# Optimization experiments

Hardware: AMD Instinct MI355X
Metric: run time of the kernel (lower is better)

Reference implementation:

```python
import math
import jax, jax.numpy as jnp
import numpy as np

B, T, DIN, D, L, H = 512, 16, 7, 512, 2, 8
FF = 4 * D
HD = D // H
NEG = -1e30


def setup_inputs() -> dict:
    key = jax.random.key(0)
    ks = jax.random.split(key, 18)
    s = 0.02
    n = lambda k, sh: jax.random.normal(k, sh, dtype=jnp.float32) * s
    return {
        "x_scalar_norm": jax.random.normal(ks[0], (B, T, DIN), dtype=jnp.float32),
        "ip_w": n(ks[1], (DIN, D)),   # input_proj (x @ W)
        "ip_b": n(ks[2], (D,)),
        "qkv_w": n(ks[3], (L, D, 3 * D)),  # packed in_proj per layer
        "qkv_b": n(ks[4], (L, 3 * D)),
        "out_w": n(ks[5], (L, D, D)),
        "out_b": n(ks[6], (L, D)),
        "ln1_s": jnp.ones((L, D), jnp.float32),
        "ln1_b": jnp.zeros((L, D), jnp.float32),
        "ff_w1": n(ks[7], (L, D, FF)),
        "ff_b1": n(ks[8], (L, FF)),
        "ff_w2": n(ks[9], (L, FF, D)),
        "ff_b2": n(ks[10], (L, D)),
        "ln2_s": jnp.ones((L, D), jnp.float32),
        "ln2_b": jnp.zeros((L, D), jnp.float32),
        "head_w": n(ks[11], (D, 3)),  # moment_head
        "head_b": n(ks[12], (3,)),
    }


def _pos_encoding(t, d):
    pos = jnp.arange(t, dtype=jnp.float32)[:, None]
    div = jnp.exp(jnp.arange(0, d, 2, dtype=jnp.float32) * (-math.log(10000.0) / d))
    pe = jnp.zeros((t, d), jnp.float32)
    pe = pe.at[:, 0::2].set(jnp.sin(pos * div))
    pe = pe.at[:, 1::2].set(jnp.cos(pos * div))
    return pe


def _ln(x, s, b, eps=1e-5):
    m = jnp.mean(x, axis=-1, keepdims=True)
    v = jnp.mean(jnp.square(x - m), axis=-1, keepdims=True)
    return (x - m) * jax.lax.rsqrt(v + eps) * s + b


def _encoder_layer(h, qkv_w, qkv_b, out_w, out_b, ln1_s, ln1_b,
                   w1, b1, w2, b2, ln2_s, ln2_b, causal):
    b, t, _ = h.shape
    qkv = h @ qkv_w + qkv_b  # [b, t, 3D]
    q, k, v = jnp.split(qkv, 3, axis=-1)
    q = q.reshape(b, t, H, HD).transpose(0, 2, 1, 3)  # bhqd
    k = k.reshape(b, t, H, HD).transpose(0, 2, 1, 3)
    v = v.reshape(b, t, H, HD).transpose(0, 2, 1, 3)
    scores = jnp.einsum('bhqd,bhkd->bhqk', q, k) / math.sqrt(HD)
    scores = jnp.where(causal[None, None], scores, NEG)
    attn = jax.nn.softmax(scores, axis=-1)
    o = jnp.einsum('bhqk,bhkd->bhqd', attn, v)
    o = o.transpose(0, 2, 1, 3).reshape(b, t, D) @ out_w + out_b
    h = _ln(h + o, ln1_s, ln1_b)           # post-norm (norm_first=False)
    ff = jax.nn.relu(h @ w1 + b1) @ w2 + b2
    return _ln(h + ff, ln2_s, ln2_b)


def reference(x_scalar_norm, ip_w, ip_b, qkv_w, qkv_b, out_w, out_b,
              ln1_s, ln1_b, ff_w1, ff_b1, ff_w2, ff_b2, ln2_s, ln2_b,
              head_w, head_b):
    b, t_total, _ = x_scalar_norm.shape
    pe = _pos_encoding(t_total, D)
    x_roll = x_scalar_norm
    preds = []
    for t in range(t_total):
        xp = x_roll[:, :t + 1, :]                 # full backbone recompute per step
        h = xp @ ip_w + ip_b + pe[None, :t + 1]
        causal = jnp.tril(jnp.ones((t + 1, t + 1), dtype=bool))
        for l in range(L):
            h = _encoder_layer(h, qkv_w[l], qkv_b[l], out_w[l], out_b[l],
                               ln1_s[l], ln1_b[l], ff_w1[l], ff_b1[l],
                               ff_w2[l], ff_b2[l], ln2_s[l], ln2_b[l], causal)
        y_t = h[:, -1, :] @ head_w + head_b       # [b, 3]
        preds.append(y_t)
        if t < t_total - 1:
            # eval mode: no teacher forcing; feed back detached prediction
            x_roll = x_roll.at[:, t + 1, DIN - 3:].set(jax.lax.stop_gradient(y_t))
    return jnp.stack(preds, axis=1)  # [b, T, 3]
```

## Files before the change

### kernel.cpp

```cpp
#include <hip/hip_runtime.h>
#include <hip/hip_bf16.h>
#include <math.h>


typedef __attribute__((__ext_vector_type__(8))) short short8;
typedef __attribute__((__ext_vector_type__(4))) float floatx4;

__device__ inline short8 as_short8(uint4 v){ union U{uint4 u; short8 s;} x; x.u=v; return x.s; }

__device__ inline ushort f2bf(float f){
    __hip_bfloat16 h = __float2bfloat16(f);
    ushort u; __builtin_memcpy(&u, &h, 2); return u;
}

__device__ inline uint32_t sld32(const void* p){
    return __hip_atomic_load((const uint32_t*)p, __ATOMIC_RELAXED, __HIP_MEMORY_SCOPE_SYSTEM);
}
__device__ inline void sst32(void* p, uint32_t v){
    __hip_atomic_store((uint32_t*)p, v, __ATOMIC_RELAXED, __HIP_MEMORY_SCOPE_SYSTEM);
}
__device__ inline unsigned long long sld64(const void* p){
    return __hip_atomic_load((const unsigned long long*)p, __ATOMIC_RELAXED, __HIP_MEMORY_SCOPE_SYSTEM);
}
__device__ inline void sst64(void* p, unsigned long long v){
    __hip_atomic_store((unsigned long long*)p, v, __ATOMIC_RELAXED, __HIP_MEMORY_SCOPE_SYSTEM);
}
__device__ inline float u2f(uint32_t u){ float f; __builtin_memcpy(&f, &u, 4); return f; }
__device__ inline uint32_t f2u(float f){ uint32_t u; __builtin_memcpy(&u, &f, 4); return u; }

#define WS_H      12582912
#define WS_TMP    13631488
#define WS_ST1    14680064
#define WS_ST2    14712832
#define WS_YPART  14745600
#define WS_BAR    14794752
#define WS_HBF    14796800
#define WS_ATTN   15321088
#define WS_FFBF   15845376
#define WS_KC     17942528
#define WS_VC     34719744

__global__ __launch_bounds__(256)
void swz_k(const float* __restrict__ qkv_w, const float* __restrict__ out_w,
           const float* __restrict__ ff1_w, const float* __restrict__ ff2_w,
           ushort* __restrict__ wsw)
{
    if (blockIdx.x == 0 && blockIdx.y == 0 && blockIdx.z == 0){
        unsigned* bar = (unsigned*)((char*)wsw + WS_BAR);
        for (int i = threadIdx.x; i < 512; i += 256)
            sst32(&bar[i], 0u);
    }
    int id = blockIdx.z; int l = id & 1; int mi = id >> 1;
    int K, N; const float* src; size_t doff;
    if (mi == 0)      { K = 512;  N = 1536; src = qkv_w + (size_t)l*786432;  doff = (size_t)l*786432; }
    else if (mi == 1) { K = 512;  N = 512;  src = out_w + (size_t)l*262144;  doff = 1572864 + (size_t)l*262144; }
    else if (mi == 2) { K = 512;  N = 2048; src = ff1_w + (size_t)l*1048576; doff = 2097152 + (size_t)l*1048576; }
    else              { K = 2048; N = 512;  src = ff2_w + (size_t)l*1048576; doff = 4194304 + (size_t)l*1048576; }
    int n0 = blockIdx.x * 64, k0 = blockIdx.y * 32;
    if (n0 >= N || k0 >= K) return;
    __shared__ float tt[32][64];
    int tid = threadIdx.x;
    int c = tid & 63, r = tid >> 6;
    #pragma unroll
    for (int i = 0; i < 8; ++i)
        tt[r + i*4][c] = src[(size_t)(k0 + r + i*4)*N + n0 + c];
    __syncthreads();
    int q = tid >> 6, n = tid & 63;
    union { ushort s[8]; uint4 v; } pk;
    #pragma unroll
    for (int i = 0; i < 8; ++i) pk.s[i] = f2bf(tt[q*8 + i][n]);
    ((uint4*)(wsw + doff))[(size_t)((k0 >> 5)*4 + q)*N + n0 + n] = pk.v;
}

#define ALDS(c, m) aLds[(((c) << 4)) + (((m) ^ ((c) & 15)))]

__global__ __launch_bounds__(512, 1)
void mega_k(const float* __restrict__ x, const float* __restrict__ ip_w,
            const float* __restrict__ ip_b, const float* __restrict__ qkv_b,
            const float* __restrict__ out_b, const float* __restrict__ ln1_s,
            const float* __restrict__ ln1_b, const float* __restrict__ ff_b1,
            const float* __restrict__ ff_b2, const float* __restrict__ ln2_s,
            const float* __restrict__ ln2_b, const float* __restrict__ hw,
            const float* __restrict__ hb, float* __restrict__ out,
            char* __restrict__ ws)
{
    const ushort* wsw = (const ushort*)ws;
    float* h     = (float*)(ws + WS_H);
    float* tmp   = (float*)(ws + WS_TMP);
    float* st1   = (float*)(ws + WS_ST1);
    float* st2   = (float*)(ws + WS_ST2);
    float* ypart = (float*)(ws + WS_YPART);
    unsigned* bar = (unsigned*)(ws + WS_BAR);
    __hip_bfloat16* hbf    = (__hip_bfloat16*)(ws + WS_HBF);
    __hip_bfloat16* attnbf = (__hip_bfloat16*)(ws + WS_ATTN);
    __hip_bfloat16* ffbf   = (__hip_bfloat16*)(ws + WS_FFBF);
    __hip_bfloat16* kc0    = (__hip_bfloat16*)(ws + WS_KC);
    __hip_bfloat16* vc0    = (__hip_bfloat16*)(ws + WS_VC);

    const int g  = blockIdx.x & 31;
    const int j  = blockIdx.x >> 5;
    const int b0 = g * 16;
    const int tid  = threadIdx.x;
    const int lane = tid & 63, w = tid >> 6;
    const int qd = lane >> 4, ln = lane & 15;
    unsigned* cnt = bar + g*16;
    unsigned epoch = 0;

    __shared__ uint4 aLds[256*16];
    __shared__ float qLds[16][68];
    __shared__ float yLds[16][3];
    __shared__ float meanLds[16], rstdLds[16];
    __shared__ float redS[4][4][4], redQ[4][4][4];
    __shared__ floatx4 fred[4][64];
    __shared__ float yred[4][16][3];

    auto gbar = [&]() {
        __syncthreads();
        epoch += 8;
        if (tid == 0){
            __hip_atomic_fetch_add(cnt, 1u, __ATOMIC_RELAXED, __HIP_MEMORY_SCOPE_SYSTEM);
            while (__hip_atomic_load(cnt, __ATOMIC_RELAXED, __HIP_MEMORY_SCOPE_SYSTEM) < epoch)
                __builtin_amdgcn_s_sleep(8);
        }
        __syncthreads();
    };

    for (int t = 0; t < 16; ++t){
        for (int l = 0; l < 2; ++l){
            __hip_bfloat16* kc = kc0 + (size_t)l*4194304;
            __hip_bfloat16* vc = vc0 + (size_t)l*4194304;

            if (l == 1){
                const unsigned long long* src = (const unsigned long long*)hbf;
                #pragma unroll
                for (int i = 0; i < 2; ++i){
                    int e = tid + i*512; int m = e >> 6, cg = e & 63;
                    size_t gi = ((size_t)(b0+m)*64 + cg)*2;
                    union { unsigned long long q[2]; uint4 v; } u;
                    u.q[0] = sld64(src + gi); u.q[1] = sld64(src + gi + 1);
                    ALDS(cg, m) = u.v;
                }
            } else {
                if (t > 0){
                    if (tid < 48){
                        int r = tid / 3, c = tid - r*3;
                        float yv = hb[c];
                        #pragma unroll
                        for (int jj = 0; jj < 8; ++jj)
                            yv += u2f(sld32(&ypart[((size_t)(b0+r)*8 + jj)*3 + c]));
                        yLds[r][c] = yv;
                        if (j == 0)
                            out[((size_t)(b0+r)*16 + (t-1))*3 + c] = yv;
                    }
                    __syncthreads();
                }
                #pragma unroll
                for (int i = 0; i < 2; ++i){
                    int e = tid + i*512; int m = e >> 6, cg = e & 63;
                    int b = b0 + m;
                    const float* xr = x + ((size_t)b*16 + t)*7;
                    float f4, f5, f6;
                    if (t == 0){ f4 = xr[4]; f5 = xr[5]; f6 = xr[6]; }
                    else { f4 = yLds[m][0]; f5 = yLds[m][1]; f6 = yLds[m][2]; }
                    float x0 = xr[0], x1 = xr[1], x2 = xr[2], x3 = xr[3];
                    float hv[8];
                    union { ushort s[8]; uint4 v; } pk;
                    #pragma unroll
                    for (int k = 0; k < 8; ++k){
                        int d = cg*8 + k;
                        int e2 = d & ~1;
                        float div = expf(-(float)e2 * (9.210340371976184f / 512.0f));
                        float arg = (float)t * div;
                        float pe = (d & 1) ? cosf(arg) : sinf(arg);
                        float acc = ip_b[d] + pe
                            + x0*ip_w[0*512+d] + x1*ip_w[1*512+d]
                            + x2*ip_w[2*512+d] + x3*ip_w[3*512+d]
                            + f4*ip_w[4*512+d] + f5*ip_w[5*512+d] + f6*ip_w[6*512+d];
                        hv[k] = acc;
                        pk.s[k] = f2bf(acc);
                    }
                    ALDS(cg, m) = pk.v;
                    if ((cg >> 3) == j){
                        float4* hp = (float4*)(h + (size_t)(b0+m)*512 + cg*8);
                        hp[0] = make_float4(hv[0],hv[1],hv[2],hv[3]);
                        hp[1] = make_float4(hv[4],hv[5],hv[6],hv[7]);
                    }
                }
            }
            __syncthreads();

            {
                const uint4* Bg = (const uint4*)(wsw + (size_t)l*786432);
                int s0 = (w < 4) ? (w >> 1) : 2;
                int cs = (w < 4) ? ((w & 1)*2) : (w - 4);
                int cN = (w < 4) ? 2 : 1;
                floatx4 acc[2] = {};
                for (int kb = 0; kb < 16; ++kb){
                    short8 af = as_short8(ALDS(kb*4 + qd, ln));
                    #pragma unroll
                    for (int c = 0; c < 2; ++c){
                        if (c < cN){
                            int n = s0*512 + j*64 + (cs + c)*16 + ln;
                            short8 bf = as_short8(Bg[(size_t)(kb*4 + qd)*1536 + n]);
                            acc[c] = __builtin_amdgcn_mfma_f32_16x16x32_bf16(af, bf, acc[c], 0, 0, 0);
                        }
                    }
                }
                #pragma unroll
                for (int c = 0; c < 2; ++c){
                    if (c < cN){
                        #pragma unroll
                        for (int r = 0; r < 4; ++r){
                            int row = qd*4 + r;
                            int cc = (cs + c)*16 + ln;
                            int n = s0*512 + j*64 + cc;
                            float v = acc[c][r] + qkv_b[l*1536 + n];
                            int b = b0 + row;
                            if (s0 == 0) qLds[row][cc] = v;
                            else if (s0 == 1) kc[(((size_t)b*8 + j)*16 + t)*64 + cc] = __float2bfloat16(v);
                            else              vc[(((size_t)b*8 + j)*16 + t)*64 + cc] = __float2bfloat16(v);
                        }
                    }
                }
            }
            __syncthreads();

            {
                #pragma unroll
                for (int i = 0; i < 2; ++i){
                    int m = w*2 + i;
                    int b = b0 + m;
                    float q = qLds[m][lane];
                    const __hip_bfloat16* kp = kc + ((size_t)b*8 + j)*1024;
                    const __hip_bfloat16* vp = vc + ((size_t)b*8 + j)*1024;
                    float mr = -1e30f, s = 0.0f, o = 0.0f;
                    for (int jj = 0; jj <= t; ++jj){
                        float p = q * __bfloat162float(kp[jj*64 + lane]);
                        #pragma unroll
                        for (int off = 32; off; off >>= 1) p += __shfl_xor(p, off);
                        p *= 0.125f;
                        float nm = fmaxf(mr, p);
                        float sc = __expf(mr - nm);
                        float e  = __expf(p - nm);
                        s = s*sc + e;
                        o = o*sc + e*__bfloat162float(vp[jj*64 + lane]);
                        mr = nm;
                    }
                    float ov = o / s;
                    float ovp = __shfl_xor(ov, 1);
                    if (!(lane & 1)){
                        uint32_t pk2 = (uint32_t)f2bf(ov) | ((uint32_t)f2bf(ovp) << 16);
                        sst32((uint32_t*)attnbf + (((size_t)b*512 + j*64 + lane) >> 1), pk2);
                    }
                }
            }
            gbar();

            {
                const unsigned long long* src = (const unsigned long long*)attnbf;
                #pragma unroll
                for (int i = 0; i < 2; ++i){
                    int e = tid + i*512; int m = e >> 6, cg = e & 63;
                    size_t gi = ((size_t)(b0+m)*64 + cg)*2;
                    union { unsigned long long q[2]; uint4 v; } u;
                    u.q[0] = sld64(src + gi); u.q[1] = sld64(src + gi + 1);
                    ALDS(cg, m) = u.v;
                }
                __syncthreads();
                if (w < 4){
                    const uint4* Bg = (const uint4*)(wsw + 1572864 + (size_t)l*262144);
                    floatx4 acc = {};
                    int nb = j*64 + w*16;
                    for (int kb = 0; kb < 16; ++kb){
                        short8 af = as_short8(ALDS(kb*4 + qd, ln));
                        short8 bf = as_short8(Bg[(size_t)(kb*4 + qd)*512 + nb + ln]);
                        acc = __builtin_amdgcn_mfma_f32_16x16x32_bf16(af, bf, acc, 0, 0, 0);
                    }
                    int n = nb + ln;
                    float psum[4], psq[4];
                    #pragma unroll
                    for (int r = 0; r < 4; ++r){
                        int row = qd*4 + r, b = b0 + row;
                        float v = acc[r] + out_b[l*512 + n] + h[(size_t)b*512 + n];
                        sst32(&tmp[(size_t)b*512 + n], f2u(v));
                        psum[r] = v; psq[r] = v*v;
                    }
                    #pragma unroll
                    for (int off = 1; off < 16; off <<= 1){
                        #pragma unroll
                        for (int r = 0; r < 4; ++r){
                            psum[r] += __shfl_xor(psum[r], off);
                            psq[r]  += __shfl_xor(psq[r],  off);
                        }
                    }
                    if (ln == 0){
                        #pragma unroll
                        for (int r = 0; r < 4; ++r){ redS[w][qd][r] = psum[r]; redQ[w][qd][r] = psq[r]; }
                    }
                }
                __syncthreads();
                if (tid < 16){
                    int q2 = tid >> 2, r2 = tid & 3;
                    float sm = redS[0][q2][r2]+redS[1][q2][r2]+redS[2][q2][r2]+redS[3][q2][r2];
                    float sq = redQ[0][q2][r2]+redQ[1][q2][r2]+redQ[2][q2][r2]+redQ[3][q2][r2];
                    union { float f[2]; unsigned long long q; } u;
                    u.f[0] = sm; u.f[1] = sq;
                    sst64(&st1[((size_t)(b0+tid)*8 + j)*2], u.q);
                }
            }
            gbar();

            {
                if (tid < 16){
                    float sm = 0.f, sq = 0.f;
                    #pragma unroll
                    for (int jj = 0; jj < 8; ++jj){
                        union { unsigned long long q; float f[2]; } u;
                        u.q = sld64(&st1[((size_t)(b0+tid)*8 + jj)*2]);
                        sm += u.f[0]; sq += u.f[1];
                    }
                    float mean = sm * (1.0f/512.0f);
                    float var  = sq * (1.0f/512.0f) - mean*mean;
                    meanLds[tid] = mean;
                    rstdLds[tid] = rsqrtf(var + 1e-5f);
                }
                __syncthreads();
                #pragma unroll
                for (int i = 0; i < 2; ++i){
                    int e = tid + i*512; int m = e >> 6, cg = e & 63;
                    int b = b0 + m;
                    float mean = meanLds[m], rs = rstdLds[m];
                    const float* tp = tmp + (size_t)b*512 + cg*8;
                    union { unsigned long long q[4]; float f[8]; } uu;
                    uu.q[0] = sld64(tp);     uu.q[1] = sld64(tp + 2);
                    uu.q[2] = sld64(tp + 4); uu.q[3] = sld64(tp + 6);
                    float hn[8];
                    union { ushort s[8]; uint4 v; } pk;
                    #pragma unroll
                    for (int k = 0; k < 8; ++k){
                        int d = cg*8 + k;
                        float nv = (uu.f[k] - mean)*rs*ln1_s[l*512 + d] + ln1_b[l*512 + d];
                        hn[k] = nv;
                        pk.s[k] = f2bf(nv);
                    }
                    ALDS(cg, m) = pk.v;
                    if ((cg >> 3) == j){
                        float4* hp = (float4*)(h + (size_t)b*512 + cg*8);
                        hp[0] = make_float4(hn[0],hn[1],hn[2],hn[3]);
                        hp[1] = make_float4(hn[4],hn[5],hn[6],hn[7]);
                    }
                }
                __syncthreads();
                const uint4* Bg = (const uint4*)(wsw + 2097152 + (size_t)l*1048576);
                floatx4 acc[2] = {};
                int nb = j*256 + w*32;
                for (int kb = 0; kb < 16; ++kb){
                    short8 af = as_short8(ALDS(kb*4 + qd, ln));
                    #pragma unroll
                    for (int c = 0; c < 2; ++c){
                        short8 bf = as_short8(Bg[(size_t)(kb*4 + qd)*2048 + nb + c*16 + ln]);
                        acc[c] = __builtin_amdgcn_mfma_f32_16x16x32_bf16(af, bf, acc[c], 0, 0, 0);
                    }
                }
                #pragma unroll
                for (int c = 0; c < 2; ++c){
                    #pragma unroll
                    for (int r = 0; r < 4; ++r){
                        int row = qd*4 + r, b = b0 + row;
                        int n = nb + c*16 + ln;
                        float v  = acc[c][r] + ff_b1[l*2048 + n];
                        float vr = fmaxf(v, 0.0f);
                        float vp = __shfl_xor(vr, 1);
                        if (!(ln & 1)){
                            uint32_t pk2 = (uint32_t)f2bf(vr) | ((uint32_t)f2bf(vp) << 16);
                            sst32((uint32_t*)ffbf + (((size_t)b*2048 + n) >> 1), pk2);
                        }
                    }
                }
            }
            gbar();

            {
                const unsigned long long* src = (const unsigned long long*)ffbf;
                unsigned long long sb[16];
                #pragma unroll
                for (int i = 0; i < 8; ++i){
                    int e = tid + i*512;
                    size_t gi = ((size_t)(b0 + (e >> 8))*256 + (e & 255))*2;
                    sb[i*2]   = sld64(src + gi);
                    sb[i*2+1] = sld64(src + gi + 1);
                }
                #pragma unroll
                for (int i = 0; i < 8; ++i){
                    int e = tid + i*512; int m = e >> 8, cg = e & 255;
                    union { unsigned long long q[2]; uint4 v; } u;
                    u.q[0] = sb[i*2]; u.q[1] = sb[i*2+1];
                    ALDS(cg, m) = u.v;
                }
                __syncthreads();
                const uint4* Bg = (const uint4*)(wsw + 4194304 + (size_t)l*1048576);
                int tw = w & 3, hf = w >> 2;
                floatx4 acc = {};
                int nb = j*64 + tw*16;
                for (int kb = hf*32; kb < hf*32 + 32; ++kb){
                    short8 af = as_short8(ALDS(kb*4 + qd, ln));
                    short8 bf = as_short8(Bg[(size_t)(kb*4 + qd)*512 + nb + ln]);
                    acc = __builtin_amdgcn_mfma_f32_16x16x32_bf16(af, bf, acc, 0, 0, 0);
                }
                if (hf == 1) fred[tw][lane] = acc;
                __syncthreads();
                if (hf == 0){
                    floatx4 a2 = fred[tw][lane];
                    acc[0] += a2[0]; acc[1] += a2[1]; acc[2] += a2[2]; acc[3] += a2[3];
                    int n = nb + ln;
                    float psum[4], psq[4];
                    #pragma unroll
                    for (int r = 0; r < 4; ++r){
                        int row = qd*4 + r, b = b0 + row;
                        float v = acc[r] + ff_b2[l*512 + n] + h[(size_t)b*512 + n];
                        sst32(&tmp[(size_t)b*512 + n], f2u(v));
                        psum[r] = v; psq[r] = v*v;
                    }
                    #pragma unroll
                    for (int off = 1; off < 16; off <<= 1){
                        #pragma unroll
                        for (int r = 0; r < 4; ++r){
                            psum[r] += __shfl_xor(psum[r], off);
                            psq[r]  += __shfl_xor(psq[r],  off);
                        }
                    }
                    if (ln == 0){
                        #pragma unroll
                        for (int r = 0; r < 4; ++r){ redS[tw][qd][r] = psum[r]; redQ[tw][qd][r] = psq[r]; }
                    }
                }
                __syncthreads();
                if (tid < 16){
                    int q2 = tid >> 2, r2 = tid & 3;
                    float sm = redS[0][q2][r2]+redS[1][q2][r2]+redS[2][q2][r2]+redS[3][q2][r2];
                    float sq = redQ[0][q2][r2]+redQ[1][q2][r2]+redQ[2][q2][r2]+redQ[3][q2][r2];
                    union { float f[2]; unsigned long long q; } u;
                    u.f[0] = sm; u.f[1] = sq;
                    sst64(&st2[((size_t)(b0+tid)*8 + j)*2], u.q);
                }
            }
            gbar();

            {
                if (tid < 16){
                    float sm = 0.f, sq = 0.f;
                    #pragma unroll
                    for (int jj = 0; jj < 8; ++jj){
                        union { unsigned long long q; float f[2]; } u;
                        u.q = sld64(&st2[((size_t)(b0+tid)*8 + jj)*2]);
                        sm += u.f[0]; sq += u.f[1];
                    }
                    float mean = sm * (1.0f/512.0f);
                    float var  = sq * (1.0f/512.0f) - mean*mean;
                    meanLds[tid] = mean;
                    rstdLds[tid] = rsqrtf(var + 1e-5f);
                }
                __syncthreads();
                if (tid < 256){
                    int r = tid >> 4, q16 = tid & 15;
                    int b = b0 + r;
                    int d0 = j*64 + q16*4;
                    const float* tp = tmp + (size_t)b*512 + d0;
                    union { unsigned long long q[2]; float f[4]; } uu;
                    uu.q[0] = sld64(tp); uu.q[1] = sld64(tp + 2);
                    float mean = meanLds[r], rs = rstdLds[r];
                    float hn0 = (uu.f[0] - mean)*rs*ln2_s[l*512 + d0+0] + ln2_b[l*512 + d0+0];
                    float hn1 = (uu.f[1] - mean)*rs*ln2_s[l*512 + d0+1] + ln2_b[l*512 + d0+1];
                    float hn2 = (uu.f[2] - mean)*rs*ln2_s[l*512 + d0+2] + ln2_b[l*512 + d0+2];
                    float hn3 = (uu.f[3] - mean)*rs*ln2_s[l*512 + d0+3] + ln2_b[l*512 + d0+3];
                    if (l == 0){
                        *(float4*)(h + (size_t)b*512 + d0) = make_float4(hn0,hn1,hn2,hn3);
                        union { ushort s[4]; unsigned long long q; } pk;
                        pk.s[0]=f2bf(hn0); pk.s[1]=f2bf(hn1); pk.s[2]=f2bf(hn2); pk.s[3]=f2bf(hn3);
                        sst64((ushort*)hbf + (size_t)b*512 + d0, pk.q);
                    } else {
                        float s0 = hn0*hw[(d0+0)*3+0] + hn1*hw[(d0+1)*3+0] + hn2*hw[(d0+2)*3+0] + hn3*hw[(d0+3)*3+0];
                        float s1 = hn0*hw[(d0+0)*3+1] + hn1*hw[(d0+1)*3+1] + hn2*hw[(d0+2)*3+1] + hn3*hw[(d0+3)*3+1];
                        float s2 = hn0*hw[(d0+0)*3+2] + hn1*hw[(d0+1)*3+2] + hn2*hw[(d0+2)*3+2] + hn3*hw[(d0+3)*3+2];
                        #pragma unroll
                        for (int off = 1; off < 16; off <<= 1){
                            s0 += __shfl_xor(s0, off);
                            s1 += __shfl_xor(s1, off);
                            s2 += __shfl_xor(s2, off);
                        }
                        if (q16 == 0){
                            yred[tid >> 6][r][0] = s0;
                            yred[tid >> 6][r][1] = s1;
                            yred[tid >> 6][r][2] = s2;
                        }
                    }
                }
                if (l == 1){
                    __syncthreads();
                    if (tid < 48){
                        int r = tid / 3, c = tid - r*3;
                        float* yp = ypart + ((size_t)(b0+r)*8 + j)*3;
                        sst32(yp + c, f2u(yred[r >> 2][r][c]));
                    }
                }
            }
            gbar();
        }
    }

    if (j == 0 && tid < 48){
        int r = tid / 3, c = tid - r*3;
        float yv = hb[c];
        #pragma unroll
        for (int jj = 0; jj < 8; ++jj)
            yv += u2f(sld32(&ypart[((size_t)(b0+r)*8 + jj)*3 + c]));
        out[((size_t)(b0+r)*16 + 15)*3 + c] = yv;
    }
}

extern "C" void kernel_launch(void* const* d_in, const int* in_sizes, int n_in,
                              void* d_out, int out_size, void* d_ws, size_t ws_size,
                              hipStream_t stream)
{
    const float* x     = (const float*)d_in[0];
    const float* ip_w  = (const float*)d_in[1];
    const float* ip_b  = (const float*)d_in[2];
    const float* qkv_w = (const float*)d_in[3];
    const float* qkv_b = (const float*)d_in[4];
    const float* out_w = (const float*)d_in[5];
    const float* out_b = (const float*)d_in[6];
    const float* ln1_s = (const float*)d_in[7];
    const float* ln1_b = (const float*)d_in[8];
    const float* ff_w1 = (const float*)d_in[9];
    const float* ff_b1 = (const float*)d_in[10];
    const float* ff_w2 = (const float*)d_in[11];
    const float* ff_b2 = (const float*)d_in[12];
    const float* ln2_s = (const float*)d_in[13];
    const float* ln2_b = (const float*)d_in[14];
    const float* hw    = (const float*)d_in[15];
    const float* hb    = (const float*)d_in[16];
    float* outp = (float*)d_out;
    char* wsc   = (char*)d_ws;

    swz_k<<<dim3(32, 64, 8), 256, 0, stream>>>(qkv_w, out_w, ff_w1, ff_w2, (ushort*)d_ws);

    mega_k<<<dim3(256), dim3(512), 0, stream>>>(
        x, ip_w, ip_b, qkv_b, out_b, ln1_s, ln1_b,
        ff_b1, ff_b2, ln2_s, ln2_b, hw, hb, outp, wsc);
}
```

Before: 2.834 ms.

## Double mega-kernel block size to 1024 threads and split work across more waves

Launches the persistent kernel with 1024 threads (16 waves) instead of 512, giving each wave one row or one MFMA tile instead of two. The out-projection and FF2 GEMMs now split the K dimension four ways with a three-slot LDS reduction, and the QKV GEMM spreads its 12 tiles over 12 waves. The goal is more latency hiding and MFMA parallelism per CU inside the grid-synchronized kernel. In exchange, register budget per thread is halved under the 1024-thread launch bound and there is more LDS reduction traffic.

```diff
diff --git a/kernel.cpp b/kernel.cpp
--- a/kernel.cpp
+++ b/kernel.cpp
@@ -74,7 +74,7 @@
 
 #define ALDS(c, m) aLds[(((c) << 4)) + (((m) ^ ((c) & 15)))]
 
-__global__ __launch_bounds__(512, 1)
+__global__ __launch_bounds__(1024, 1)
 void mega_k(const float* __restrict__ x, const float* __restrict__ ip_w,
             const float* __restrict__ ip_b, const float* __restrict__ qkv_b,
             const float* __restrict__ out_b, const float* __restrict__ ln1_s,
@@ -111,7 +111,7 @@
     __shared__ float yLds[16][3];
     __shared__ float meanLds[16], rstdLds[16];
     __shared__ float redS[4][4][4], redQ[4][4][4];
-    __shared__ floatx4 fred[4][64];
+    __shared__ floatx4 fred[4][3][64];
     __shared__ float yred[4][16][3];
 
     auto gbar = [&]() {
@@ -132,14 +132,11 @@
 
             if (l == 1){
                 const unsigned long long* src = (const unsigned long long*)hbf;
-                #pragma unroll
-                for (int i = 0; i < 2; ++i){
-                    int e = tid + i*512; int m = e >> 6, cg = e & 63;
-                    size_t gi = ((size_t)(b0+m)*64 + cg)*2;
-                    union { unsigned long long q[2]; uint4 v; } u;
-                    u.q[0] = sld64(src + gi); u.q[1] = sld64(src + gi + 1);
-                    ALDS(cg, m) = u.v;
-                }
+                int m = tid >> 6, cg = tid & 63;
+                size_t gi = ((size_t)(b0+m)*64 + cg)*2;
+                union { unsigned long long q[2]; uint4 v; } u;
+                u.q[0] = sld64(src + gi); u.q[1] = sld64(src + gi + 1);
+                ALDS(cg, m) = u.v;
             } else {
                 if (t > 0){
                     if (tid < 48){
@@ -154,127 +151,118 @@
                     }
                     __syncthreads();
                 }
+                int m = tid >> 6, cg = tid & 63;
+                int b = b0 + m;
+                const float* xr = x + ((size_t)b*16 + t)*7;
+                float f4, f5, f6;
+                if (t == 0){ f4 = xr[4]; f5 = xr[5]; f6 = xr[6]; }
+                else { f4 = yLds[m][0]; f5 = yLds[m][1]; f6 = yLds[m][2]; }
+                float x0 = xr[0], x1 = xr[1], x2 = xr[2], x3 = xr[3];
+                float hv[8];
+                union { ushort s[8]; uint4 v; } pk;
                 #pragma unroll
-                for (int i = 0; i < 2; ++i){
-                    int e = tid + i*512; int m = e >> 6, cg = e & 63;
-                    int b = b0 + m;
-                    const float* xr = x + ((size_t)b*16 + t)*7;
-                    float f4, f5, f6;
-                    if (t == 0){ f4 = xr[4]; f5 = xr[5]; f6 = xr[6]; }
-                    else { f4 = yLds[m][0]; f5 = yLds[m][1]; f6 = yLds[m][2]; }
-                    float x0 = xr[0], x1 = xr[1], x2 = xr[2], x3 = xr[3];
-                    float hv[8];
-                    union { ushort s[8]; uint4 v; } pk;
-                    #pragma unroll
-                    for (int k = 0; k < 8; ++k){
-                        int d = cg*8 + k;
-                        int e2 = d & ~1;
-                        float div = expf(-(float)e2 * (9.210340371976184f / 512.0f));
-                        float arg = (float)t * div;
-                        float pe = (d & 1) ? cosf(arg) : sinf(arg);
-                        float acc = ip_b[d] + pe
-                            + x0*ip_w[0*512+d] + x1*ip_w[1*512+d]
-                            + x2*ip_w[2*512+d] + x3*ip_w[3*512+d]
-                            + f4*ip_w[4*512+d] + f5*ip_w[5*512+d] + f6*ip_w[6*512+d];
-                        hv[k] = acc;
-                        pk.s[k] = f2bf(acc);
-                    }
-                    ALDS(cg, m) = pk.v;
-                    if ((cg >> 3) == j){
-                        float4* hp = (float4*)(h + (size_t)(b0+m)*512 + cg*8);
-                        hp[0] = make_float4(hv[0],hv[1],hv[2],hv[3]);
-                        hp[1] = make_float4(hv[4],hv[5],hv[6],hv[7]);
-                    }
+                for (int k = 0; k < 8; ++k){
+                    int d = cg*8 + k;
+                    int e2 = d & ~1;
+                    float div = expf(-(float)e2 * (9.210340371976184f / 512.0f));
+                    float arg = (float)t * div;
+                    float pe = (d & 1) ? cosf(arg) : sinf(arg);
+                    float acc = ip_b[d] + pe
+                        + x0*ip_w[0*512+d] + x1*ip_w[1*512+d]
+                        + x2*ip_w[2*512+d] + x3*ip_w[3*512+d]
+                        + f4*ip_w[4*512+d] + f5*ip_w[5*512+d] + f6*ip_w[6*512+d];
+                    hv[k] = acc;
+                    pk.s[k] = f2bf(acc);
+                }
+                ALDS(cg, m) = pk.v;
+                if ((cg >> 3) == j){
+                    float4* hp = (float4*)(h + (size_t)b*512 + cg*8);
+                    hp[0] = make_float4(hv[0],hv[1],hv[2],hv[3]);
+                    hp[1] = make_float4(hv[4],hv[5],hv[6],hv[7]);
                 }
             }
             __syncthreads();
 
             {
-                const uint4* Bg = (const uint4*)(wsw + (size_t)l*786432);
-                int s0 = (w < 4) ? (w >> 1) : 2;
-                int cs = (w < 4) ? ((w & 1)*2) : (w - 4);
-                int cN = (w < 4) ? 2 : 1;
-                floatx4 acc[2] = {};
-                for (int kb = 0; kb < 16; ++kb){
-                    short8 af = as_short8(ALDS(kb*4 + qd, ln));
-                    #pragma unroll
-                    for (int c = 0; c < 2; ++c){
-                        if (c < cN){
-                            int n = s0*512 + j*64 + (cs + c)*16 + ln;
-                            short8 bf = as_short8(Bg[(size_t)(kb*4 + qd)*1536 + n]);
-                            acc[c] = __builtin_amdgcn_mfma_f32_16x16x32_bf16(af, bf, acc[c], 0, 0, 0);
-                        }
-                    }
-                }
-                #pragma unroll
-                for (int c = 0; c < 2; ++c){
-                    if (c < cN){
-                        #pragma unroll
-                        for (int r = 0; r < 4; ++r){
-                            int row = qd*4 + r;
-                            int cc = (cs + c)*16 + ln;
-                            int n = s0*512 + j*64 + cc;
-                            float v = acc[c][r] + qkv_b[l*1536 + n];
-                            int b = b0 + row;
-                            if (s0 == 0) qLds[row][cc] = v;
-                            else if (s0 == 1) kc[(((size_t)b*8 + j)*16 + t)*64 + cc] = __float2bfloat16(v);
-                            else              vc[(((size_t)b*8 + j)*16 + t)*64 + cc] = __float2bfloat16(v);
-                        }
+                if (w < 12){
+                    const uint4* Bg = (const uint4*)(wsw + (size_t)l*786432);
+                    int s0 = w >> 2, cs = w & 3;
+                    floatx4 acc = {};
+                    for (int kb = 0; kb < 16; ++kb){
+                        short8 af = as_short8(ALDS(kb*4 + qd, ln));
+                        int n = s0*512 + j*64 + cs*16 + ln;
+                        short8 bf = as_short8(Bg[(size_t)(kb*4 + qd)*1536 + n]);
+                        acc = __builtin_amdgcn_mfma_f32_16x16x32_bf16(af, bf, acc, 0, 0, 0);
+                    }
+                    #pragma unroll
+                    for (int r = 0; r < 4; ++r){
+                        int row = qd*4 + r;
+                        int cc = cs*16 + ln;
+                        int n = s0*512 + j*64 + cc;
+                        float v = acc[r] + qkv_b[l*1536 + n];
+                        int b = b0 + row;
+                        if (s0 == 0) qLds[row][cc] = v;
+                        else if (s0 == 1) kc[(((size_t)b*8 + j)*16 + t)*64 + cc] = __float2bfloat16(v);
+                        else              vc[(((size_t)b*8 + j)*16 + t)*64 + cc] = __float2bfloat16(v);
                     }
                 }
             }
             __syncthreads();
 
             {
-                #pragma unroll
-                for (int i = 0; i < 2; ++i){
-                    int m = w*2 + i;
-                    int b = b0 + m;
-                    float q = qLds[m][lane];
-                    const __hip_bfloat16* kp = kc + ((size_t)b*8 + j)*1024;
-                    const __hip_bfloat16* vp = vc + ((size_t)b*8 + j)*1024;
-                    float mr = -1e30f, s = 0.0f, o = 0.0f;
-                    for (int jj = 0; jj <= t; ++jj){
-                        float p = q * __bfloat162float(kp[jj*64 + lane]);
-                        #pragma unroll
-                        for (int off = 32; off; off >>= 1) p += __shfl_xor(p, off);
-                        p *= 0.125f;
-                        float nm = fmaxf(mr, p);
-                        float sc = __expf(mr - nm);
-                        float e  = __expf(p - nm);
-                        s = s*sc + e;
-                        o = o*sc + e*__bfloat162float(vp[jj*64 + lane]);
-                        mr = nm;
-                    }
-                    float ov = o / s;
-                    float ovp = __shfl_xor(ov, 1);
-                    if (!(lane & 1)){
-                        uint32_t pk2 = (uint32_t)f2bf(ov) | ((uint32_t)f2bf(ovp) << 16);
-                        sst32((uint32_t*)attnbf + (((size_t)b*512 + j*64 + lane) >> 1), pk2);
-                    }
+                int m = w;
+                int b = b0 + m;
+                float q = qLds[m][lane];
+                const __hip_bfloat16* kp = kc + ((size_t)b*8 + j)*1024;
+                const __hip_bfloat16* vp = vc + ((size_t)b*8 + j)*1024;
+                float mr = -1e30f, s = 0.0f, o = 0.0f;
+                for (int jj = 0; jj <= t; ++jj){
+                    float p = q * __bfloat162float(kp[jj*64 + lane]);
+                    #pragma unroll
+                    for (int off = 32; off; off >>= 1) p += __shfl_xor(p, off);
+                    p *= 0.125f;
+                    float nm = fmaxf(mr, p);
+                    float sc = __expf(mr - nm);
+                    float e  = __expf(p - nm);
+                    s = s*sc + e;
+                    o = o*sc + e*__bfloat162float(vp[jj*64 + lane]);
+                    mr = nm;
+                }
+                float ov = o / s;
+                float ovp = __shfl_xor(ov, 1);
+                if (!(lane & 1)){
+                    uint32_t pk2 = (uint32_t)f2bf(ov) | ((uint32_t)f2bf(ovp) << 16);
+                    sst32((uint32_t*)attnbf + (((size_t)b*512 + j*64 + lane) >> 1), pk2);
                 }
             }
             gbar();
 
             {
                 const unsigned long long* src = (const unsigned long long*)attnbf;
-                #pragma unroll
-                for (int i = 0; i < 2; ++i){
-                    int e = tid + i*512; int m = e >> 6, cg = e & 63;
+                {
+                    int m = tid >> 6, cg = tid & 63;
                     size_t gi = ((size_t)(b0+m)*64 + cg)*2;
                     union { unsigned long long q[2]; uint4 v; } u;
                     u.q[0] = sld64(src + gi); u.q[1] = sld64(src + gi + 1);
                     ALDS(cg, m) = u.v;
                 }
                 __syncthreads();
-                if (w < 4){
-                    const uint4* Bg = (const uint4*)(wsw + 1572864 + (size_t)l*262144);
-                    floatx4 acc = {};
-                    int nb = j*64 + w*16;
-                    for (int kb = 0; kb < 16; ++kb){
-                        short8 af = as_short8(ALDS(kb*4 + qd, ln));
-                        short8 bf = as_short8(Bg[(size_t)(kb*4 + qd)*512 + nb + ln]);
-                        acc = __builtin_amdgcn_mfma_f32_16x16x32_bf16(af, bf, acc, 0, 0, 0);
+                const uint4* Bg = (const uint4*)(wsw + 1572864 + (size_t)l*262144);
+                int tw = w >> 2, hf = w & 3;
+                floatx4 acc = {};
+                int nb = j*64 + tw*16;
+                for (int kb = hf*4; kb < hf*4 + 4; ++kb){
+                    short8 af = as_short8(ALDS(kb*4 + qd, ln));
+                    short8 bf = as_short8(Bg[(size_t)(kb*4 + qd)*512 + nb + ln]);
+                    acc = __builtin_amdgcn_mfma_f32_16x16x32_bf16(af, bf, acc, 0, 0, 0);
+                }
+                if (hf) fred[tw][hf-1][lane] = acc;
+                __syncthreads();
+                if (hf == 0){
+                    #pragma unroll
+                    for (int q2 = 0; q2 < 3; ++q2){
+                        floatx4 a2 = fred[tw][q2][lane];
+                        acc[0] += a2[0]; acc[1] += a2[1]; acc[2] += a2[2]; acc[3] += a2[3];
                     }
                     int n = nb + ln;
                     float psum[4], psq[4];
@@ -295,7 +283,7 @@
                     }
                     if (ln == 0){
                         #pragma unroll
-                        for (int r = 0; r < 4; ++r){ redS[w][qd][r] = psum[r]; redQ[w][qd][r] = psq[r]; }
+                        for (int r = 0; r < 4; ++r){ redS[tw][qd][r] = psum[r]; redQ[tw][qd][r] = psq[r]; }
                     }
                 }
                 __syncthreads();
@@ -325,9 +313,8 @@
                     rstdLds[tid] = rsqrtf(var + 1e-5f);
                 }
                 __syncthreads();
-                #pragma unroll
-                for (int i = 0; i < 2; ++i){
-                    int e = tid + i*512; int m = e >> 6, cg = e & 63;
+                {
+                    int m = tid >> 6, cg = tid & 63;
                     int b = b0 + m;
                     float mean = meanLds[m], rs = rstdLds[m];
                     const float* tp = tmp + (size_t)b*512 + cg*8;
@@ -352,29 +339,23 @@
                 }
                 __syncthreads();
                 const uint4* Bg = (const uint4*)(wsw + 2097152 + (size_t)l*1048576);
-                floatx4 acc[2] = {};
-                int nb = j*256 + w*32;
+                floatx4 acc = {};
+                int nb = j*256 + w*16;
                 for (int kb = 0; kb < 16; ++kb){
                     short8 af = as_short8(ALDS(kb*4 + qd, ln));
-                    #pragma unroll
-                    for (int c = 0; c < 2; ++c){
-                        short8 bf = as_short8(Bg[(size_t)(kb*4 + qd)*2048 + nb + c*16 + ln]);
-                        acc[c] = __builtin_amdgcn_mfma_f32_16x16x32_bf16(af, bf, acc[c], 0, 0, 0);
-                    }
+                    short8 bf = as_short8(Bg[(size_t)(kb*4 + qd)*2048 + nb + ln]);
+                    acc = __builtin_amdgcn_mfma_f32_16x16x32_bf16(af, bf, acc, 0, 0, 0);
                 }
                 #pragma unroll
-                for (int c = 0; c < 2; ++c){
-                    #pragma unroll
-                    for (int r = 0; r < 4; ++r){
-                        int row = qd*4 + r, b = b0 + row;
-                        int n = nb + c*16 + ln;
-                        float v  = acc[c][r] + ff_b1[l*2048 + n];
-                        float vr = fmaxf(v, 0.0f);
-                        float vp = __shfl_xor(vr, 1);
-                        if (!(ln & 1)){
-                            uint32_t pk2 = (uint32_t)f2bf(vr) | ((uint32_t)f2bf(vp) << 16);
-                            sst32((uint32_t*)ffbf + (((size_t)b*2048 + n) >> 1), pk2);
-                        }
+                for (int r = 0; r < 4; ++r){
+                    int row = qd*4 + r, b = b0 + row;
+                    int n = nb + ln;
+                    float v  = acc[r] + ff_b1[l*2048 + n];
+                    float vr = fmaxf(v, 0.0f);
+                    float vp = __shfl_xor(vr, 1);
+                    if (!(ln & 1)){
+                        uint32_t pk2 = (uint32_t)f2bf(vr) | ((uint32_t)f2bf(vp) << 16);
+                        sst32((uint32_t*)ffbf + (((size_t)b*2048 + n) >> 1), pk2);
                     }
                 }
             }
@@ -382,36 +363,39 @@
 
             {
                 const unsigned long long* src = (const unsigned long long*)ffbf;
-                unsigned long long sb[16];
+                unsigned long long sb[8];
                 #pragma unroll
-                for (int i = 0; i < 8; ++i){
-                    int e = tid + i*512;
+                for (int i = 0; i < 4; ++i){
+                    int e = tid + i*1024;
                     size_t gi = ((size_t)(b0 + (e >> 8))*256 + (e & 255))*2;
                     sb[i*2]   = sld64(src + gi);
                     sb[i*2+1] = sld64(src + gi + 1);
                 }
                 #pragma unroll
-                for (int i = 0; i < 8; ++i){
-                    int e = tid + i*512; int m = e >> 8, cg = e & 255;
+                for (int i = 0; i < 4; ++i){
+                    int e = tid + i*1024; int m = e >> 8, cg = e & 255;
                     union { unsigned long long q[2]; uint4 v; } u;
                     u.q[0] = sb[i*2]; u.q[1] = sb[i*2+1];
                     ALDS(cg, m) = u.v;
                 }
                 __syncthreads();
                 const uint4* Bg = (const uint4*)(wsw + 4194304 + (size_t)l*1048576);
-                int tw = w & 3, hf = w >> 2;
+                int tw = w >> 2, hf = w & 3;
                 floatx4 acc = {};
                 int nb = j*64 + tw*16;
-                for (int kb = hf*32; kb < hf*32 + 32; ++kb){
+                for (int kb = hf*16; kb < hf*16 + 16; ++kb){
                     short8 af = as_short8(ALDS(kb*4 + qd, ln));
                     short8 bf = as_short8(Bg[(size_t)(kb*4 + qd)*512 + nb + ln]);
                     acc = __builtin_amdgcn_mfma_f32_16x16x32_bf16(af, bf, acc, 0, 0, 0);
                 }
-                if (hf == 1) fred[tw][lane] = acc;
+                if (hf) fred[tw][hf-1][lane] = acc;
                 __syncthreads();
                 if (hf == 0){
-                    floatx4 a2 = fred[tw][lane];
-                    acc[0] += a2[0]; acc[1] += a2[1]; acc[2] += a2[2]; acc[3] += a2[3];
+                    #pragma unroll
+                    for (int q2 = 0; q2 < 3; ++q2){
+                        floatx4 a2 = fred[tw][q2][lane];
+                        acc[0] += a2[0]; acc[1] += a2[1]; acc[2] += a2[2]; acc[3] += a2[3];
+                    }
                     int n = nb + ln;
                     float psum[4], psq[4];
                     #pragma unroll
@@ -544,7 +528,7 @@
 
     swz_k<<<dim3(32, 64, 8), 256, 0, stream>>>(qkv_w, out_w, ff_w1, ff_w2, (ushort*)d_ws);
 
-    mega_k<<<dim3(256), dim3(512), 0, stream>>>(
+    mega_k<<<dim3(256), dim3(1024), 0, stream>>>(
         x, ip_w, ip_b, qkv_b, out_b, ln1_s, ln1_b,
         ff_b1, ff_b2, ln2_s, ln2_b, hw, hb, outp, wsc);
 }
```

Result: faster. 2.561 ms (-9.7%).
